# Kernel optimization log

Hardware: AMD Instinct MI355X
Metric: run time of the kernel (lower is better)

## Reference

```python
import jax, jax.numpy as jnp
import numpy as np
from jax import lax

BLOCK = 20  # hardcoded block_size in BlockSparseSelfAttention
HEADS = 8
LAYERS = 4
EPS = 1e-5


def _ln(x, g, b):
    m = jnp.mean(x, axis=-1, keepdims=True)
    v = jnp.mean(jnp.square(x - m), axis=-1, keepdims=True)
    return (x - m) * lax.rsqrt(v + EPS) * g + b


def _conv1d(x_nct, w, b):
    # x: (B,C,T), w: (O,I,3) -> (B,O,T), padding=1 == SAME for k=3
    y = lax.conv_general_dilated(x_nct, w, (1,), 'SAME',
                                 dimension_numbers=('NCH', 'OIH', 'NCH'))
    return y + b[None, :, None]


def _block_attn(x, in_w, in_b, out_w, out_b):
    # torch nn.MultiheadAttention applied independently per length-BLOCK chunk
    B, T, D = x.shape
    nb, hd = T // BLOCK, D // HEADS
    xb = x.reshape(B, nb, BLOCK, D)
    qkv = jnp.einsum('bnsd,ed->bnse', xb, in_w) + in_b  # e = 3D
    q, k, v = jnp.split(qkv, 3, axis=-1)
    q = q.reshape(B, nb, BLOCK, HEADS, hd)
    k = k.reshape(B, nb, BLOCK, HEADS, hd)
    v = v.reshape(B, nb, BLOCK, HEADS, hd)
    scale = jnp.asarray(1.0 / np.sqrt(hd), x.dtype)
    s = jnp.einsum('bnqhd,bnkhd->bnhqk', q, k) * scale
    a = jax.nn.softmax(s, axis=-1)
    o = jnp.einsum('bnhqk,bnkhd->bnqhd', a, v).reshape(B, nb, BLOCK, D)
    o = jnp.einsum('bnsd,od->bnso', o, out_w) + out_b
    return o.reshape(B, T, D)


def setup_inputs() -> dict:
    key = jax.random.key(0)
    ks = iter(jax.random.split(key, 16))
    B, T, C, D, L = 32, 4000, 16, 256, LAYERS
    F = 4 * D
    s_c = 1.0 / np.sqrt(C * 3)
    s_d = 1.0 / np.sqrt(D)
    s_d3 = 1.0 / np.sqrt(D * 3)
    s_f = 1.0 / np.sqrt(F)
    f32 = jnp.float32
    return {
        'x': jax.random.normal(next(ks), (B, T, C), f32),
        'conv1_w': jax.random.normal(next(ks), (D, C, 3), f32) * s_c,
        'conv1_b': jnp.zeros((D,), f32),
        'conv2_w': jax.random.normal(next(ks), (D, D, 3), f32) * s_d3,
        'conv2_b': jnp.zeros((D,), f32),
        'ln_f_g': jnp.ones((D,), f32), 'ln_f_b': jnp.zeros((D,), f32),
        'trend_w': jax.random.normal(next(ks), (D, D), f32) * s_d,
        'trend_b': jnp.zeros((D,), f32),
        'season_w': jax.random.normal(next(ks), (D, D), f32) * s_d,
        'season_b': jnp.zeros((D,), f32),
        'attn_in_w': jax.random.normal(next(ks), (L, 3 * D, D), f32) * s_d,
        'attn_in_b': jnp.zeros((L, 3 * D), f32),
        'attn_out_w': jax.random.normal(next(ks), (L, D, D), f32) * s_d,
        'attn_out_b': jnp.zeros((L, D), f32),
        'ln1_g': jnp.ones((L, D), f32), 'ln1_b': jnp.zeros((L, D), f32),
        'ff1_w': jax.random.normal(next(ks), (L, F, D), f32) * s_d,
        'ff1_b': jnp.zeros((L, F), f32),
        'ff2_w': jax.random.normal(next(ks), (L, D, F), f32) * s_f,
        'ff2_b': jnp.zeros((L, D), f32),
        'ln2_g': jnp.ones((L, D), f32), 'ln2_b': jnp.zeros((L, D), f32),
        'fc_w': jax.random.normal(next(ks), (C, D), f32) * s_d,
        'fc_b': jnp.zeros((C,), f32),
    }


def reference(x, conv1_w, conv1_b, conv2_w, conv2_b, ln_f_g, ln_f_b,
              trend_w, trend_b, season_w, season_b,
              attn_in_w, attn_in_b, attn_out_w, attn_out_b,
              ln1_g, ln1_b, ff1_w, ff1_b, ff2_w, ff2_b, ln2_g, ln2_b,
              fc_w, fc_b):
    # FeatureExtractor
    h = x.transpose(0, 2, 1)                       # (B,C,T)
    h = jax.nn.relu(_conv1d(h, conv1_w, conv1_b))
    h = jax.nn.relu(_conv1d(h, conv2_w, conv2_b))
    h = h.transpose(0, 2, 1)                       # (B,T,D)
    h = _ln(h, ln_f_g, ln_f_b)
    # trend + seasonality residual
    h = h + (h @ trend_w.T + trend_b) + jnp.sin(h @ season_w.T + season_b)
    # encoder stack (dropout disabled / eval mode)
    for i in range(LAYERS):
        a = _block_attn(h, attn_in_w[i], attn_in_b[i], attn_out_w[i], attn_out_b[i])
        h = _ln(h + a, ln1_g[i], ln1_b[i])
        f = jax.nn.relu(h @ ff1_w[i].T + ff1_b[i]) @ ff2_w[i].T + ff2_b[i]
        h = _ln(h + f, ln2_g[i], ln2_b[i])
    return h[:, -1, :] @ fc_w.T + fc_b             # (B,C)
```

## Files before the change

kernel.cpp:

```cpp
#include <hip/hip_runtime.h>
#include <math.h>

typedef __attribute__((ext_vector_type(8))) short short8;
typedef __attribute__((ext_vector_type(4))) short short4v;
typedef __attribute__((ext_vector_type(4))) float f32x4;
typedef unsigned short ushort;
typedef unsigned int uint;
typedef unsigned long long u64;

#define MFMA16(a, b, c) __builtin_amdgcn_mfma_f32_16x16x32_bf16(a, b, c, 0, 0, 0)

__device__ __forceinline__ ushort f2bf(float f) {
  uint u = __float_as_uint(f);
  u = (u + 0x7FFFu + ((u >> 16) & 1u)) >> 16;
  return (ushort)u;
}
__device__ __forceinline__ int swz(int idx, int sh) {
  return idx ^ (((idx >> sh) & 7) << 3);
}
__device__ __forceinline__ float wsum(float v) {
#pragma unroll
  for (int off = 32; off > 0; off >>= 1) v += __shfl_xor(v, off, 64);
  return v;
}
__device__ __forceinline__ void gload16(short8& dst, const ushort* g) {
  u64 ga = (u64)g;
  asm volatile("global_load_dwordx4 %0, %1, off" : "=v"(dst) : "v"(ga));
}
__device__ __forceinline__ void vmw(int n) {
  if (n >= 7) asm volatile("s_waitcnt vmcnt(7)" ::: "memory");
  else if (n == 6) asm volatile("s_waitcnt vmcnt(6)" ::: "memory");
  else if (n == 5) asm volatile("s_waitcnt vmcnt(5)" ::: "memory");
  else if (n == 4) asm volatile("s_waitcnt vmcnt(4)" ::: "memory");
  else if (n == 3) asm volatile("s_waitcnt vmcnt(3)" ::: "memory");
  else if (n == 2) asm volatile("s_waitcnt vmcnt(2)" ::: "memory");
  else if (n == 1) asm volatile("s_waitcnt vmcnt(1)" ::: "memory");
  else asm volatile("s_waitcnt vmcnt(0)" ::: "memory");
}

#define S_CONV2 0
#define S_TREND 196608
#define S_SEASON 262144
#define S_QKV 327680
#define S_AOW 1114112
#define S_F1 1376256
#define S_F2 2424832
#define WTOT 3473408
#define O_C2O 3653632
#define O_G0 3981312
#define O_G1 4308992
#define O_PEND 4636672
#define O_QKV 4964352
#define O_FFB 5455872

template <int NCH>
__device__ __forceinline__ void dec2(int idx, int& row, int& k) {
  int pos = idx & 511, lane = pos >> 3, j = pos & 7;
  int kg = lane >> 4, col = lane & 15;
  int chunk = idx >> 9;
  int tile = chunk / (NCH * 4), r = chunk - tile * (NCH * 4);
  int kc = r >> 2, ks = r & 3;
  row = tile * 16 + col;
  k = kc * 128 + ks * 32 + kg * 8 + j;
}

__global__ void k_cvt(const float* __restrict__ c2w, const float* __restrict__ tw,
                      const float* __restrict__ sw, const float* __restrict__ aiw,
                      const float* __restrict__ aow, const float* __restrict__ f1w,
                      const float* __restrict__ f2w, ushort* __restrict__ ws) {
  for (int i = blockIdx.x * blockDim.x + threadIdx.x; i < WTOT;
       i += gridDim.x * blockDim.x) {
    float v; int row, k;
    if (i < S_TREND) {
      dec2<6>(i, row, k);
      int t = k >> 8, e = k & 255;
      v = c2w[row * 768 + e * 3 + t];
    } else if (i < S_SEASON) { dec2<2>(i - S_TREND, row, k); v = tw[row * 256 + k]; }
    else if (i < S_QKV) { dec2<2>(i - S_SEASON, row, k); v = sw[row * 256 + k]; }
    else if (i < S_AOW) {
      int r = i - S_QKV; int l = r / 196608; r -= l * 196608;
      dec2<2>(r, row, k); v = aiw[(size_t)l * 196608 + row * 256 + k];
    } else if (i < S_F1) {
      int r = i - S_AOW; int l = r >> 16; r &= 65535;
      dec2<2>(r, row, k); v = aow[l * 65536 + row * 256 + k];
    } else if (i < S_F2) {
      int r = i - S_F1; int l = r >> 18; r &= 262143;
      dec2<2>(r, row, k); v = f1w[l * 262144 + row * 256 + k];
    } else {
      int r = i - S_F2; int l = r >> 18; r &= 262143;
      dec2<8>(r, row, k); v = f2w[l * 262144 + row * 1024 + k];
    }
    ws[i] = f2bf(v);
  }
}

template <int NCH, int MY, int ASH>
__device__ __forceinline__ void ring_gemm(const ushort* __restrict__ A, int lda,
                                          const ushort* __restrict__ ws0,
                                          int lane, f32x4 (&acc)[MY][2]) {
  constexpr int C = MY * NCH * 4;
  constexpr int R = (C < 8) ? C : 8;
  const int col = lane & 15, kg = lane >> 4;
  const int r1c = (16 + col > 19) ? 19 : (16 + col);
  short8 rg[R];
#pragma unroll
  for (int r = 0; r < R; ++r) gload16(rg[r], ws0 + r * 512);
  short8 af0[4], af1[4];
#pragma unroll
  for (int c = 0; c < C; ++c) {
    const int i = c / (NCH * 4), r = c - i * (NCH * 4);
    const int kc = r >> 2, ks = r & 3;
    if (ks == 0) {
#pragma unroll
      for (int s = 0; s < 4; ++s) {
        const int k0 = kc * 128 + s * 32 + kg * 8;
        af0[s] = *(const short8*)(A + swz(col * lda + k0, ASH));
        af1[s] = *(const short8*)(A + swz(r1c * lda + k0, ASH));
      }
    }
    int allow = C - 1 - c; if (allow > R - 1) allow = R - 1;
    vmw(allow);
    __builtin_amdgcn_sched_barrier(0);
    acc[i][0] = MFMA16(af0[ks], rg[c % R], acc[i][0]);
    acc[i][1] = MFMA16(af1[ks], rg[c % R], acc[i][1]);
    if (c + R < C) gload16(rg[c % R], ws0 + (c + R) * 512);
  }
}

__device__ __forceinline__ void stage_b16(const ushort* __restrict__ g, ushort* hb,
                                          int n, int sh, int tid) {
  for (int i = tid * 8; i < n; i += 2048) {
    short8 v = *(const short8*)(g + i);
    *(short8*)(hb + swz(i, sh)) = v;
  }
}
__device__ __forceinline__ void stage_f32(const float* __restrict__ g, ushort* hb, int tid) {
  for (int i = tid * 8; i < 5120; i += 2048) {
    float4 a = *(const float4*)(g + i);
    float4 b = *(const float4*)(g + i + 4);
    short8 t;
    t[0] = f2bf(a.x); t[1] = f2bf(a.y); t[2] = f2bf(a.z); t[3] = f2bf(a.w);
    t[4] = f2bf(b.x); t[5] = f2bf(b.y); t[6] = f2bf(b.z); t[7] = f2bf(b.w);
    *(short8*)(hb + swz(i, 8)) = t;
  }
}
__device__ __forceinline__ void stage_ln(const float* __restrict__ g1,
                                         const float* __restrict__ pend,
                                         const float* __restrict__ gam,
                                         const float* __restrict__ bet,
                                         ushort* hb, float* __restrict__ gout,
                                         float* f32lds, int tid) {
  const int lane = tid & 63, w = tid >> 6, d0 = lane * 4;
  for (int r = w; r < 20; r += 4) {
    float4 a = *(const float4*)(g1 + r * 256 + d0);
    if (pend) {
      float4 p = *(const float4*)(pend + r * 256 + d0);
      a.x += p.x; a.y += p.y; a.z += p.z; a.w += p.w;
    }
    float m = wsum(a.x + a.y + a.z + a.w) * (1.f / 256.f);
    float c0 = a.x - m, c1 = a.y - m, c2 = a.z - m, c3 = a.w - m;
    float var = wsum(c0 * c0 + c1 * c1 + c2 * c2 + c3 * c3) * (1.f / 256.f);
    float inv = rsqrtf(var + 1e-5f);
    float o0 = c0 * inv * gam[d0] + bet[d0];
    float o1 = c1 * inv * gam[d0 + 1] + bet[d0 + 1];
    float o2 = c2 * inv * gam[d0 + 2] + bet[d0 + 2];
    float o3 = c3 * inv * gam[d0 + 3] + bet[d0 + 3];
    short4v t; t[0] = f2bf(o0); t[1] = f2bf(o1); t[2] = f2bf(o2); t[3] = f2bf(o3);
    *(short4v*)(hb + swz(r * 256 + d0, 8)) = t;
    if (gout) { float4 o = {o0, o1, o2, o3}; *(float4*)(gout + r * 256 + d0) = o; }
    if (f32lds) { float4 o = {o0, o1, o2, o3}; *(float4*)(f32lds + r * 256 + d0) = o; }
  }
}

__global__ __launch_bounds__(256, 2) void k_conv12(
    const float* __restrict__ x, const float* __restrict__ c1w,
    const float* __restrict__ c1b, const ushort* __restrict__ wst,
    const float* __restrict__ c2b, float* __restrict__ c2o) {
  __shared__ float xs[24][16];
  __shared__ __align__(16) ushort c1u[5632];
  const int tid = threadIdx.x, lane = tid & 63, wv = tid >> 6;
  const int b = blockIdx.x >> 2, slice = blockIdx.x & 3;
  const int col = lane & 15, kg = lane >> 4;
  for (int i = tid; i < 24 * 16; i += 256) {
    int r = i >> 4, c = i & 15;
    xs[r][c] = (r < 23) ? x[((size_t)b * 4000 + 3977 + r) * 16 + c] : 0.f;
  }
  __syncthreads();
  {
    const int d = tid;
    const float* wr = c1w + d * 48;
    float acc[21];
    const float bv = c1b[d];
#pragma unroll
    for (int r = 0; r < 21; ++r) acc[r] = bv;
    for (int c = 0; c < 16; ++c) {
      float xv[23];
#pragma unroll
      for (int i = 0; i < 23; ++i) xv[i] = xs[i + 1][c];
      float w0 = wr[c * 3], w1 = wr[c * 3 + 1], w2 = wr[c * 3 + 2];
#pragma unroll
      for (int r = 0; r < 21; ++r)
        acc[r] += xv[r] * w0 + xv[r + 1] * w1 + xv[r + 2] * w2;
    }
#pragma unroll
    for (int r = 0; r < 21; ++r)
      c1u[swz(r * 256 + d, 8)] = f2bf(fmaxf(acc[r], 0.f));
    c1u[swz(21 * 256 + d, 8)] = 0;
  }
  const int tile = slice * 4 + wv, og = tile * 16 + col;
  float bv2 = c2b[og];
  __syncthreads();
  asm volatile("s_waitcnt vmcnt(0)" ::: "memory");
  f32x4 acc2[1][2];
  acc2[0][0] = {bv2, bv2, bv2, bv2}; acc2[0][1] = {bv2, bv2, bv2, bv2};
  ring_gemm<6, 1, 8>(c1u, 256, wst + tile * 12288 + lane * 8, lane, acc2);
  float* ob = c2o + b * 5120;
#pragma unroll
  for (int mt = 0; mt < 2; ++mt)
#pragma unroll
    for (int j = 0; j < 4; ++j) {
      int row = mt * 16 + kg * 4 + j;
      if (row < 20) ob[row * 256 + og] = fmaxf(acc2[0][mt][j], 0.f);
    }
}

__global__ __launch_bounds__(256, 2) void k_tresea(
    const float* __restrict__ c2o, const ushort* __restrict__ wtr,
    const ushort* __restrict__ wse, const float* __restrict__ lnfg,
    const float* __restrict__ lnfb, const float* __restrict__ tb,
    const float* __restrict__ sb, float* __restrict__ g0) {
  __shared__ __align__(16) ushort hb[5120];
  __shared__ float hf[5120];
  const int tid = threadIdx.x, lane = tid & 63, wv = tid >> 6;
  const int b = blockIdx.x >> 2, slice = blockIdx.x & 3;
  const int col = lane & 15, kg = lane >> 4;
  stage_ln(c2o + b * 5120, nullptr, lnfg, lnfb, hb, nullptr, hf, tid);
  const int tile = slice * 4 + wv, og = tile * 16 + col;
  float bt = tb[og], bs = sb[og];
  __syncthreads();
  asm volatile("s_waitcnt vmcnt(0)" ::: "memory");
  f32x4 at[1][2], as_[1][2];
  at[0][0] = {bt, bt, bt, bt}; at[0][1] = {bt, bt, bt, bt};
  as_[0][0] = {bs, bs, bs, bs}; as_[0][1] = {bs, bs, bs, bs};
  ring_gemm<2, 1, 8>(hb, 256, wtr + tile * 4096 + lane * 8, lane, at);
  ring_gemm<2, 1, 8>(hb, 256, wse + tile * 4096 + lane * 8, lane, as_);
  float* ob = g0 + b * 5120;
#pragma unroll
  for (int mt = 0; mt < 2; ++mt)
#pragma unroll
    for (int j = 0; j < 4; ++j) {
      int row = mt * 16 + kg * 4 + j;
      if (row < 20)
        ob[row * 256 + og] = hf[row * 256 + og] + at[0][mt][j] + sinf(as_[0][mt][j]);
    }
}

__global__ __launch_bounds__(256, 2) void k_qkv(
    const float* __restrict__ gin, const float* __restrict__ pend,
    const float* __restrict__ lng, const float* __restrict__ lnb, int fuse_ln,
    float* __restrict__ gout, const ushort* __restrict__ wst,
    const float* __restrict__ bias, ushort* __restrict__ qkvo) {
  __shared__ __align__(16) ushort hb[5120];
  const int tid = threadIdx.x, lane = tid & 63, wv = tid >> 6;
  const int b = blockIdx.x / 12, slice = blockIdx.x % 12;
  const int col = lane & 15, kg = lane >> 4;
  if (fuse_ln)
    stage_ln(gin + b * 5120, pend + b * 5120, lng, lnb, hb,
             (slice == 0) ? (gout + b * 5120) : nullptr, nullptr, tid);
  else
    stage_f32(gin + b * 5120, hb, tid);
  const int tile = slice * 4 + wv, og = tile * 16 + col;
  float bv = bias[og];
  __syncthreads();
  asm volatile("s_waitcnt vmcnt(0)" ::: "memory");
  f32x4 acc[1][2];
  acc[0][0] = {bv, bv, bv, bv}; acc[0][1] = {bv, bv, bv, bv};
  ring_gemm<2, 1, 8>(hb, 256, wst + tile * 4096 + lane * 8, lane, acc);
  ushort* ob = qkvo + b * 15360;
#pragma unroll
  for (int mt = 0; mt < 2; ++mt)
#pragma unroll
    for (int j = 0; j < 4; ++j) {
      int row = mt * 16 + kg * 4 + j;
      if (row < 20) ob[row * 768 + og] = f2bf(acc[0][mt][j]);
    }
}

__global__ __launch_bounds__(256, 1) void k_aff1(
    const ushort* __restrict__ qkvo, const ushort* __restrict__ waow,
    const float* __restrict__ aobb, const float* __restrict__ g0,
    const float* __restrict__ l1g, const float* __restrict__ l1b,
    float* __restrict__ g1, const ushort* __restrict__ wf1,
    const float* __restrict__ f1b, ushort* __restrict__ ffbo) {
  __shared__ __align__(16) ushort qb[15360];
  __shared__ __align__(16) ushort vT[8192];
  __shared__ __align__(16) ushort Pb[5120];
  __shared__ __align__(16) ushort aob[5120];
  __shared__ float sc[3200];
  __shared__ __align__(16) ushort hb[5120];
  float* proj = (float*)qb;
  const int tid = threadIdx.x, lane = tid & 63, wv = tid >> 6;
  const int b = blockIdx.x >> 3, slice = blockIdx.x & 7;
  const int col = lane & 15, kg = lane >> 4;
  const int r1c = (16 + col > 19) ? 19 : (16 + col);

  stage_b16(qkvo + b * 15360, qb, 15360, 8, tid);
  __syncthreads();
  for (int i = tid; i < 8192; i += 256) {
    int hh = i >> 10, rem = i & 1023, dh = rem >> 5, tk = rem & 31;
    ushort v = (tk < 20) ? qb[swz(tk * 768 + 512 + hh * 32 + dh, 8)] : (ushort)0;
    vT[swz(i, 5)] = v;
  }
  __syncthreads();
  for (int hh = wv; hh < 8; hh += 4) {
    short8 aq[2], bk[2];
    aq[0] = *(const short8*)(qb + swz(col * 768 + hh * 32 + kg * 8, 8));
    aq[1] = *(const short8*)(qb + swz(r1c * 768 + hh * 32 + kg * 8, 8));
    bk[0] = *(const short8*)(qb + swz(col * 768 + 256 + hh * 32 + kg * 8, 8));
    bk[1] = *(const short8*)(qb + swz(r1c * 768 + 256 + hh * 32 + kg * 8, 8));
    f32x4 d[2][2];
#pragma unroll
    for (int mt = 0; mt < 2; ++mt)
#pragma unroll
      for (int nt = 0; nt < 2; ++nt) {
        d[mt][nt] = {0.f, 0.f, 0.f, 0.f};
        d[mt][nt] = MFMA16(aq[mt], bk[nt], d[mt][nt]);
      }
#pragma unroll
    for (int mt = 0; mt < 2; ++mt)
#pragma unroll
      for (int nt = 0; nt < 2; ++nt)
#pragma unroll
        for (int j = 0; j < 4; ++j) {
          int row = mt * 16 + kg * 4 + j, kj = nt * 16 + col;
          if (row < 20 && kj < 20)
            sc[hh * 400 + row * 20 + kj] = d[mt][nt][j] * 0.17677669529663687f;
        }
  }
  __syncthreads();
  if (tid < 160) {
    const int hh = tid / 20, q = tid - hh * 20;
    const float* row = sc + hh * 400 + q * 20;
    float m = row[0];
#pragma unroll
    for (int j = 1; j < 20; ++j) m = fmaxf(m, row[j]);
    float e[20], s = 0.f;
#pragma unroll
    for (int j = 0; j < 20; ++j) { e[j] = __expf(row[j] - m); s += e[j]; }
    float inv = 1.f / s;
#pragma unroll
    for (int j = 0; j < 20; ++j) Pb[swz(hh * 640 + q * 32 + j, 5)] = f2bf(e[j] * inv);
#pragma unroll
    for (int j = 20; j < 32; ++j) Pb[swz(hh * 640 + q * 32 + j, 5)] = 0;
  }
  __syncthreads();
  for (int hh = wv; hh < 8; hh += 4) {
    short8 ap[2], bvv[2];
    ap[0] = *(const short8*)(Pb + swz(hh * 640 + col * 32 + kg * 8, 5));
    ap[1] = *(const short8*)(Pb + swz(hh * 640 + r1c * 32 + kg * 8, 5));
    bvv[0] = *(const short8*)(vT + swz(hh * 1024 + col * 32 + kg * 8, 5));
    bvv[1] = *(const short8*)(vT + swz(hh * 1024 + (16 + col) * 32 + kg * 8, 5));
    f32x4 d[2][2];
#pragma unroll
    for (int mt = 0; mt < 2; ++mt)
#pragma unroll
      for (int nt = 0; nt < 2; ++nt) {
        d[mt][nt] = {0.f, 0.f, 0.f, 0.f};
        d[mt][nt] = MFMA16(ap[mt], bvv[nt], d[mt][nt]);
      }
#pragma unroll
    for (int mt = 0; mt < 2; ++mt)
#pragma unroll
      for (int nt = 0; nt < 2; ++nt)
#pragma unroll
        for (int j = 0; j < 4; ++j) {
          int row = mt * 16 + kg * 4 + j, dc = nt * 16 + col;
          if (row < 20) aob[swz(row * 256 + hh * 32 + dc, 8)] = f2bf(d[mt][nt][j]);
        }
  }
  __syncthreads();

  {
    float bo[4];
#pragma unroll
    for (int i = 0; i < 4; ++i) bo[i] = aobb[(wv * 4 + i) * 16 + col];
    asm volatile("s_waitcnt vmcnt(0)" ::: "memory");
    f32x4 acc[4][2];
#pragma unroll
    for (int i = 0; i < 4; ++i) {
      acc[i][0] = {bo[i], bo[i], bo[i], bo[i]};
      acc[i][1] = {bo[i], bo[i], bo[i], bo[i]};
    }
    ring_gemm<2, 4, 8>(aob, 256, waow + (wv * 4) * 4096 + lane * 8, lane, acc);
#pragma unroll
    for (int i = 0; i < 4; ++i) {
      const int og = (wv * 4 + i) * 16 + col;
#pragma unroll
      for (int mt = 0; mt < 2; ++mt)
#pragma unroll
        for (int j = 0; j < 4; ++j) {
          int row = mt * 16 + kg * 4 + j;
          if (row < 20) proj[row * 256 + og] = acc[i][mt][j];
        }
    }
  }
  __syncthreads();

  {
    const int d0 = lane * 4;
    for (int r = wv; r < 20; r += 4) {
      float4 a = *(const float4*)(g0 + b * 5120 + r * 256 + d0);
      a.x += proj[r * 256 + d0];
      a.y += proj[r * 256 + d0 + 1];
      a.z += proj[r * 256 + d0 + 2];
      a.w += proj[r * 256 + d0 + 3];
      float m = wsum(a.x + a.y + a.z + a.w) * (1.f / 256.f);
      float c0 = a.x - m, c1 = a.y - m, c2 = a.z - m, c3 = a.w - m;
      float var = wsum(c0 * c0 + c1 * c1 + c2 * c2 + c3 * c3) * (1.f / 256.f);
      float inv = rsqrtf(var + 1e-5f);
      float o0 = c0 * inv * l1g[d0] + l1b[d0];
      float o1 = c1 * inv * l1g[d0 + 1] + l1b[d0 + 1];
      float o2 = c2 * inv * l1g[d0 + 2] + l1b[d0 + 2];
      float o3 = c3 * inv * l1g[d0 + 3] + l1b[d0 + 3];
      short4v t; t[0] = f2bf(o0); t[1] = f2bf(o1); t[2] = f2bf(o2); t[3] = f2bf(o3);
      *(short4v*)(hb + swz(r * 256 + d0, 8)) = t;
      if (slice == 0) {
        float4 o = {o0, o1, o2, o3};
        *(float4*)(g1 + b * 5120 + r * 256 + d0) = o;
      }
    }
  }
  __syncthreads();

  {
    const int t0 = slice * 8 + wv * 2;
    float bf0 = f1b[t0 * 16 + col], bf1 = f1b[(t0 + 1) * 16 + col];
    asm volatile("s_waitcnt vmcnt(0)" ::: "memory");
    f32x4 acc[2][2];
    acc[0][0] = {bf0, bf0, bf0, bf0}; acc[0][1] = {bf0, bf0, bf0, bf0};
    acc[1][0] = {bf1, bf1, bf1, bf1}; acc[1][1] = {bf1, bf1, bf1, bf1};
    ring_gemm<2, 2, 8>(hb, 256, wf1 + t0 * 4096 + lane * 8, lane, acc);
    ushort* ob = ffbo + b * 20480;
#pragma unroll
    for (int i = 0; i < 2; ++i) {
      const int og = (t0 + i) * 16 + col;
#pragma unroll
      for (int mt = 0; mt < 2; ++mt)
#pragma unroll
        for (int j = 0; j < 4; ++j) {
          int row = mt * 16 + kg * 4 + j;
          if (row < 20) ob[row * 1024 + og] = f2bf(fmaxf(acc[i][mt][j], 0.f));
        }
    }
  }
}

__global__ __launch_bounds__(256, 2) void k_ff2(const ushort* __restrict__ ffbo,
                                                const ushort* __restrict__ wst,
                                                const float* __restrict__ bias,
                                                float* __restrict__ pend) {
  __shared__ __align__(16) ushort hb[20480];
  const int tid = threadIdx.x, lane = tid & 63, wv = tid >> 6;
  const int b = blockIdx.x >> 2, slice = blockIdx.x & 3;
  const int col = lane & 15, kg = lane >> 4;
  stage_b16(ffbo + b * 20480, hb, 20480, 10, tid);
  const int tile = slice * 4 + wv, og = tile * 16 + col;
  float bv = bias[og];
  __syncthreads();
  asm volatile("s_waitcnt vmcnt(0)" ::: "memory");
  f32x4 acc[1][2];
  acc[0][0] = {bv, bv, bv, bv}; acc[0][1] = {bv, bv, bv, bv};
  ring_gemm<8, 1, 10>(hb, 1024, wst + tile * 16384 + lane * 8, lane, acc);
  float* ob = pend + b * 5120;
#pragma unroll
  for (int mt = 0; mt < 2; ++mt)
#pragma unroll
    for (int j = 0; j < 4; ++j) {
      int row = mt * 16 + kg * 4 + j;
      if (row < 20) ob[row * 256 + og] = acc[0][mt][j];
    }
}

__global__ __launch_bounds__(256) void k_fc(
    const float* __restrict__ g1, const float* __restrict__ pend,
    const float* __restrict__ lng, const float* __restrict__ lnb,
    const float* __restrict__ fcw, const float* __restrict__ fcb,
    float* __restrict__ out) {
  __shared__ float hn[256];
  const int tid = threadIdx.x, b = blockIdx.x;
  if (tid < 64) {
    const int d0 = tid * 4;
    float4 a = *(const float4*)(g1 + b * 5120 + 19 * 256 + d0);
    float4 p = *(const float4*)(pend + b * 5120 + 19 * 256 + d0);
    a.x += p.x; a.y += p.y; a.z += p.z; a.w += p.w;
    float m = wsum(a.x + a.y + a.z + a.w) * (1.f / 256.f);
    float c0 = a.x - m, c1 = a.y - m, c2 = a.z - m, c3 = a.w - m;
    float var = wsum(c0 * c0 + c1 * c1 + c2 * c2 + c3 * c3) * (1.f / 256.f);
    float inv = rsqrtf(var + 1e-5f);
    hn[d0] = c0 * inv * lng[d0] + lnb[d0];
    hn[d0 + 1] = c1 * inv * lng[d0 + 1] + lnb[d0 + 1];
    hn[d0 + 2] = c2 * inv * lng[d0 + 2] + lnb[d0 + 2];
    hn[d0 + 3] = c3 * inv * lng[d0 + 3] + lnb[d0 + 3];
  }
  __syncthreads();
  const int g = tid >> 4, t = tid & 15;
  float s = 0.f;
#pragma unroll
  for (int j = 0; j < 16; ++j) {
    int k = t * 16 + j;
    s += hn[k] * fcw[g * 256 + k];
  }
#pragma unroll
  for (int off = 1; off < 16; off <<= 1) s += __shfl_xor(s, off, 64);
  if (t == 0) out[b * 16 + g] = s + fcb[g];
}

extern "C" void kernel_launch(void* const* d_in, const int* in_sizes, int n_in,
                              void* d_out, int out_size, void* d_ws, size_t ws_size,
                              hipStream_t stream) {
  const float* x    = (const float*)d_in[0];
  const float* c1w  = (const float*)d_in[1];
  const float* c1b  = (const float*)d_in[2];
  const float* c2w  = (const float*)d_in[3];
  const float* c2b  = (const float*)d_in[4];
  const float* lnfg = (const float*)d_in[5];
  const float* lnfb = (const float*)d_in[6];
  const float* tw   = (const float*)d_in[7];
  const float* tb   = (const float*)d_in[8];
  const float* sw   = (const float*)d_in[9];
  const float* sb   = (const float*)d_in[10];
  const float* aiw  = (const float*)d_in[11];
  const float* aib  = (const float*)d_in[12];
  const float* aow  = (const float*)d_in[13];
  const float* aobb = (const float*)d_in[14];
  const float* l1g  = (const float*)d_in[15];
  const float* l1b  = (const float*)d_in[16];
  const float* f1w  = (const float*)d_in[17];
  const float* f1b  = (const float*)d_in[18];
  const float* f2w  = (const float*)d_in[19];
  const float* f2b  = (const float*)d_in[20];
  const float* l2g  = (const float*)d_in[21];
  const float* l2b  = (const float*)d_in[22];
  const float* fcw  = (const float*)d_in[23];
  const float* fcb  = (const float*)d_in[24];
  float* out = (float*)d_out;
  ushort* ws = (ushort*)d_ws;

  float* c2o   = (float*)(ws + O_C2O);
  float* g0    = (float*)(ws + O_G0);
  float* g1    = (float*)(ws + O_G1);
  float* pend  = (float*)(ws + O_PEND);
  ushort* qkvo = ws + O_QKV;
  ushort* ffbo = ws + O_FFB;

  k_cvt<<<4096, 256, 0, stream>>>(c2w, tw, sw, aiw, aow, f1w, f2w, ws);
  k_conv12<<<128, 256, 0, stream>>>(x, c1w, c1b, ws + S_CONV2, c2b, c2o);
  k_tresea<<<128, 256, 0, stream>>>(c2o, ws + S_TREND, ws + S_SEASON, lnfg,
                                    lnfb, tb, sb, g0);
  for (int l = 0; l < 4; ++l) {
    k_qkv<<<384, 256, 0, stream>>>(
        l == 0 ? g0 : g1, pend, l ? l2g + (l - 1) * 256 : nullptr,
        l ? l2b + (l - 1) * 256 : nullptr, l ? 1 : 0, g0,
        ws + S_QKV + l * 196608, aib + l * 768, qkvo);
    k_aff1<<<256, 256, 0, stream>>>(qkvo, ws + S_AOW + l * 65536,
                                    aobb + l * 256, g0, l1g + l * 256,
                                    l1b + l * 256, g1, ws + S_F1 + l * 262144,
                                    f1b + l * 1024, ffbo);
    k_ff2<<<128, 256, 0, stream>>>(ffbo, ws + S_F2 + l * 262144, f2b + l * 256,
                                   pend);
  }
  k_fc<<<32, 256, 0, stream>>>(g1, pend, l2g + 3 * 256, l2b + 3 * 256, fcw,
                               fcb, out);
}
```

Measured before the change: 149.3 us.

## Prefetch GEMM weight rings at kernel entry to overlap activation staging

Splits ring_gemm into a prologue that issues the weight loads and a consume phase that runs the MFMAs. Each kernel now issues its weight prefetch at entry, before it stages activations, LayerNorm or attention, and drops the explicit vmcnt(0) waits. The ring depth grows to 12 in several kernels, vmw is extended up to vmcnt(15), and the k_cvt grid is halved. The aim is to hide global weight-load latency behind the staging work. The cost is more live VGPRs (k_aff1 holds two rings across the attention phase) and more fragile vmcnt bookkeeping.

```diff
diff --git a/kernel.cpp b/kernel.cpp
--- a/kernel.cpp
+++ b/kernel.cpp
@@ -28,7 +28,15 @@
   asm volatile("global_load_dwordx4 %0, %1, off" : "=v"(dst) : "v"(ga));
 }
 __device__ __forceinline__ void vmw(int n) {
-  if (n >= 7) asm volatile("s_waitcnt vmcnt(7)" ::: "memory");
+  if (n >= 15) asm volatile("s_waitcnt vmcnt(15)" ::: "memory");
+  else if (n == 14) asm volatile("s_waitcnt vmcnt(14)" ::: "memory");
+  else if (n == 13) asm volatile("s_waitcnt vmcnt(13)" ::: "memory");
+  else if (n == 12) asm volatile("s_waitcnt vmcnt(12)" ::: "memory");
+  else if (n == 11) asm volatile("s_waitcnt vmcnt(11)" ::: "memory");
+  else if (n == 10) asm volatile("s_waitcnt vmcnt(10)" ::: "memory");
+  else if (n == 9) asm volatile("s_waitcnt vmcnt(9)" ::: "memory");
+  else if (n == 8) asm volatile("s_waitcnt vmcnt(8)" ::: "memory");
+  else if (n == 7) asm volatile("s_waitcnt vmcnt(7)" ::: "memory");
   else if (n == 6) asm volatile("s_waitcnt vmcnt(6)" ::: "memory");
   else if (n == 5) asm volatile("s_waitcnt vmcnt(5)" ::: "memory");
   else if (n == 4) asm volatile("s_waitcnt vmcnt(4)" ::: "memory");
@@ -94,17 +102,21 @@
   }
 }
 
-template <int NCH, int MY, int ASH>
-__device__ __forceinline__ void ring_gemm(const ushort* __restrict__ A, int lda,
-                                          const ushort* __restrict__ ws0,
-                                          int lane, f32x4 (&acc)[MY][2]) {
+template <int R, int C>
+__device__ __forceinline__ void ring_pro(const ushort* ws0, short8* rg) {
+#pragma unroll
+  for (int r = 0; r < R; ++r) gload16(rg[r], ws0 + r * 512);
+}
+
+template <int NCH, int MY, int ASH, int R>
+__device__ __forceinline__ void ring_consume(const ushort* __restrict__ A,
+                                             int lda,
+                                             const ushort* __restrict__ ws0,
+                                             short8* rg, int lane,
+                                             f32x4 (&acc)[MY][2]) {
   constexpr int C = MY * NCH * 4;
-  constexpr int R = (C < 8) ? C : 8;
   const int col = lane & 15, kg = lane >> 4;
   const int r1c = (16 + col > 19) ? 19 : (16 + col);
-  short8 rg[R];
-#pragma unroll
-  for (int r = 0; r < R; ++r) gload16(rg[r], ws0 + r * 512);
   short8 af0[4], af1[4];
 #pragma unroll
   for (int c = 0; c < C; ++c) {
@@ -181,6 +193,10 @@
   const int tid = threadIdx.x, lane = tid & 63, wv = tid >> 6;
   const int b = blockIdx.x >> 2, slice = blockIdx.x & 3;
   const int col = lane & 15, kg = lane >> 4;
+  const int tile = slice * 4 + wv, og = tile * 16 + col;
+  const ushort* ws0 = wst + tile * 12288 + lane * 8;
+  short8 rg[12];
+  ring_pro<12, 24>(ws0, rg);
   for (int i = tid; i < 24 * 16; i += 256) {
     int r = i >> 4, c = i & 15;
     xs[r][c] = (r < 23) ? x[((size_t)b * 4000 + 3977 + r) * 16 + c] : 0.f;
@@ -207,13 +223,11 @@
       c1u[swz(r * 256 + d, 8)] = f2bf(fmaxf(acc[r], 0.f));
     c1u[swz(21 * 256 + d, 8)] = 0;
   }
-  const int tile = slice * 4 + wv, og = tile * 16 + col;
   float bv2 = c2b[og];
   __syncthreads();
-  asm volatile("s_waitcnt vmcnt(0)" ::: "memory");
   f32x4 acc2[1][2];
   acc2[0][0] = {bv2, bv2, bv2, bv2}; acc2[0][1] = {bv2, bv2, bv2, bv2};
-  ring_gemm<6, 1, 8>(c1u, 256, wst + tile * 12288 + lane * 8, lane, acc2);
+  ring_consume<6, 1, 8, 12>(c1u, 256, ws0, rg, lane, acc2);
   float* ob = c2o + b * 5120;
 #pragma unroll
   for (int mt = 0; mt < 2; ++mt)
@@ -234,16 +248,20 @@
   const int tid = threadIdx.x, lane = tid & 63, wv = tid >> 6;
   const int b = blockIdx.x >> 2, slice = blockIdx.x & 3;
   const int col = lane & 15, kg = lane >> 4;
+  const int tile = slice * 4 + wv, og = tile * 16 + col;
+  const ushort* wt0 = wtr + tile * 4096 + lane * 8;
+  const ushort* ws0 = wse + tile * 4096 + lane * 8;
+  short8 rgt[8], rgs[8];
+  ring_pro<8, 8>(wt0, rgt);
+  ring_pro<8, 8>(ws0, rgs);
   stage_ln(c2o + b * 5120, nullptr, lnfg, lnfb, hb, nullptr, hf, tid);
-  const int tile = slice * 4 + wv, og = tile * 16 + col;
   float bt = tb[og], bs = sb[og];
   __syncthreads();
-  asm volatile("s_waitcnt vmcnt(0)" ::: "memory");
   f32x4 at[1][2], as_[1][2];
   at[0][0] = {bt, bt, bt, bt}; at[0][1] = {bt, bt, bt, bt};
   as_[0][0] = {bs, bs, bs, bs}; as_[0][1] = {bs, bs, bs, bs};
-  ring_gemm<2, 1, 8>(hb, 256, wtr + tile * 4096 + lane * 8, lane, at);
-  ring_gemm<2, 1, 8>(hb, 256, wse + tile * 4096 + lane * 8, lane, as_);
+  ring_consume<2, 1, 8, 8>(hb, 256, wt0, rgt, lane, at);
+  ring_consume<2, 1, 8, 8>(hb, 256, ws0, rgs, lane, as_);
   float* ob = g0 + b * 5120;
 #pragma unroll
   for (int mt = 0; mt < 2; ++mt)
@@ -264,18 +282,20 @@
   const int tid = threadIdx.x, lane = tid & 63, wv = tid >> 6;
   const int b = blockIdx.x / 12, slice = blockIdx.x % 12;
   const int col = lane & 15, kg = lane >> 4;
+  const int tile = slice * 4 + wv, og = tile * 16 + col;
+  const ushort* ws0 = wst + tile * 4096 + lane * 8;
+  short8 rg[8];
+  ring_pro<8, 8>(ws0, rg);
   if (fuse_ln)
     stage_ln(gin + b * 5120, pend + b * 5120, lng, lnb, hb,
              (slice == 0) ? (gout + b * 5120) : nullptr, nullptr, tid);
   else
     stage_f32(gin + b * 5120, hb, tid);
-  const int tile = slice * 4 + wv, og = tile * 16 + col;
   float bv = bias[og];
   __syncthreads();
-  asm volatile("s_waitcnt vmcnt(0)" ::: "memory");
   f32x4 acc[1][2];
   acc[0][0] = {bv, bv, bv, bv}; acc[0][1] = {bv, bv, bv, bv};
-  ring_gemm<2, 1, 8>(hb, 256, wst + tile * 4096 + lane * 8, lane, acc);
+  ring_consume<2, 1, 8, 8>(hb, 256, ws0, rg, lane, acc);
   ushort* ob = qkvo + b * 15360;
 #pragma unroll
   for (int mt = 0; mt < 2; ++mt)
@@ -304,6 +324,14 @@
   const int col = lane & 15, kg = lane >> 4;
   const int r1c = (16 + col > 19) ? 19 : (16 + col);
 
+  const ushort* wo0 = waow + (wv * 4) * 4096 + lane * 8;
+  short8 rgo[12];
+  ring_pro<12, 32>(wo0, rgo);
+  const int t0 = slice * 8 + wv * 2;
+  const ushort* wf0 = wf1 + t0 * 4096 + lane * 8;
+  short8 rgf[8];
+  ring_pro<8, 8>(wf0, rgf);
+
   stage_b16(qkvo + b * 15360, qb, 15360, 8, tid);
   __syncthreads();
   for (int i = tid; i < 8192; i += 256) {
@@ -384,14 +412,13 @@
     float bo[4];
 #pragma unroll
     for (int i = 0; i < 4; ++i) bo[i] = aobb[(wv * 4 + i) * 16 + col];
-    asm volatile("s_waitcnt vmcnt(0)" ::: "memory");
     f32x4 acc[4][2];
 #pragma unroll
     for (int i = 0; i < 4; ++i) {
       acc[i][0] = {bo[i], bo[i], bo[i], bo[i]};
       acc[i][1] = {bo[i], bo[i], bo[i], bo[i]};
     }
-    ring_gemm<2, 4, 8>(aob, 256, waow + (wv * 4) * 4096 + lane * 8, lane, acc);
+    ring_consume<2, 4, 8, 12>(aob, 256, wo0, rgo, lane, acc);
 #pragma unroll
     for (int i = 0; i < 4; ++i) {
       const int og = (wv * 4 + i) * 16 + col;
@@ -433,13 +460,11 @@
   __syncthreads();
 
   {
-    const int t0 = slice * 8 + wv * 2;
     float bf0 = f1b[t0 * 16 + col], bf1 = f1b[(t0 + 1) * 16 + col];
-    asm volatile("s_waitcnt vmcnt(0)" ::: "memory");
     f32x4 acc[2][2];
     acc[0][0] = {bf0, bf0, bf0, bf0}; acc[0][1] = {bf0, bf0, bf0, bf0};
     acc[1][0] = {bf1, bf1, bf1, bf1}; acc[1][1] = {bf1, bf1, bf1, bf1};
-    ring_gemm<2, 2, 8>(hb, 256, wf1 + t0 * 4096 + lane * 8, lane, acc);
+    ring_consume<2, 2, 8, 8>(hb, 256, wf0, rgf, lane, acc);
     ushort* ob = ffbo + b * 20480;
 #pragma unroll
     for (int i = 0; i < 2; ++i) {
@@ -463,14 +488,16 @@
   const int tid = threadIdx.x, lane = tid & 63, wv = tid >> 6;
   const int b = blockIdx.x >> 2, slice = blockIdx.x & 3;
   const int col = lane & 15, kg = lane >> 4;
+  const int tile = slice * 4 + wv, og = tile * 16 + col;
+  const ushort* ws0 = wst + tile * 16384 + lane * 8;
+  short8 rg[12];
+  ring_pro<12, 32>(ws0, rg);
   stage_b16(ffbo + b * 20480, hb, 20480, 10, tid);
-  const int tile = slice * 4 + wv, og = tile * 16 + col;
   float bv = bias[og];
   __syncthreads();
-  asm volatile("s_waitcnt vmcnt(0)" ::: "memory");
   f32x4 acc[1][2];
   acc[0][0] = {bv, bv, bv, bv}; acc[0][1] = {bv, bv, bv, bv};
-  ring_gemm<8, 1, 10>(hb, 1024, wst + tile * 16384 + lane * 8, lane, acc);
+  ring_consume<8, 1, 10, 12>(hb, 1024, ws0, rg, lane, acc);
   float* ob = pend + b * 5120;
 #pragma unroll
   for (int mt = 0; mt < 2; ++mt)
@@ -553,7 +580,7 @@
   ushort* qkvo = ws + O_QKV;
   ushort* ffbo = ws + O_FFB;
 
-  k_cvt<<<4096, 256, 0, stream>>>(c2w, tw, sw, aiw, aow, f1w, f2w, ws);
+  k_cvt<<<2048, 256, 0, stream>>>(c2w, tw, sw, aiw, aow, f1w, f2w, ws);
   k_conv12<<<128, 256, 0, stream>>>(x, c1w, c1b, ws + S_CONV2, c2b, c2o);
   k_tresea<<<128, 256, 0, stream>>>(c2o, ws + S_TREND, ws + S_SEASON, lnfg,
                                     lnfb, tb, sb, g0);
```

New measurement: 149.9 us. Within noise of the previous version (+0.4%).
